# Optimization experiments

Measured on AMD Instinct MI355X. Metric: run time of the kernel, lower is better.

Reference implementation:

```python
import jax, jax.numpy as jnp
import numpy as np

# Model dims
B, S, D = 1, 768, 256          # batch, seq_len, d_model
H, KD = 8, 256                 # num_heads, key_dim
DH = KD // H                   # head_dim = 32
BS, NR, W, G = 64, 3, 3, 1     # block_size, num_rand_blocks, window_size, global_tokens
NEG = -1e9


def _build_sparse_indices(seed=0):
    """Replicates _create_sparse_attention_mask (sparse branch) with numpy.
    Returns (attn_indices [S, M] int32 clamped >=0, blocked_mask [1,1,S,M] float32)."""
    nb = S // BS  # num_blocks (S divisible by BS here)
    rng = np.random.RandomState(seed)
    r = np.arange(nb)
    # window pairs |i - j| <= W
    ii, jj = np.meshgrid(r, r, indexing='ij')
    win = np.abs(ii - jj) <= W
    window_pairs = np.stack([ii[win], jj[win]], axis=1)
    # global: every block -> first G blocks; first G blocks -> every block
    g = np.arange(G)
    glob_to = np.stack([np.repeat(r, G), np.tile(g, nb)], axis=1)
    glob_from = np.stack([np.repeat(g, nb), np.tile(r, G)], axis=1)
    # random pairs
    rand_pairs = rng.randint(0, nb, size=(NR * nb, 2))
    allp = np.concatenate([window_pairs, glob_to, glob_from, rand_pairs], axis=0)
    uniq = np.unique(allp[:, 0] * nb + allp[:, 1])  # sorted unique (row, col)
    rows, cols = uniq // nb, uniq % nb
    max_row = int(np.max(np.bincount(rows, minlength=nb)))
    M = max_row * BS  # padded neighbor-token width (= S when a global block is dense)
    idx = np.full((nb, M), -1, dtype=np.int64)
    for b in range(nb):
        cs = cols[rows == b]
        toks = (cs[:, None] * BS + np.arange(BS)[None, :]).reshape(-1)
        idx[b, :toks.size] = toks
    tok_idx = idx[np.arange(S) // BS]  # expand per-block rows to per-token rows [S, M]
    mask = np.where(tok_idx >= 0, 0.0, NEG).astype(np.float32)
    return np.maximum(tok_idx, 0).astype(np.int32), mask[None, None]


def setup_inputs() -> dict:
    key = jax.random.key(0)
    ks = jax.random.split(key, 8)

    def dense_w(k, fi, fo):  # glorot-uniform like keras Dense
        lim = float(np.sqrt(6.0 / (fi + fo)))
        return jax.random.uniform(k, (fi, fo), jnp.float32, -lim, lim)

    attn_indices, blocked_mask = _build_sparse_indices()
    return {
        'query': jax.random.normal(ks[0], (B, S, D), jnp.float32),
        'value': jax.random.normal(ks[1], (B, S, D), jnp.float32),
        'key_in': jax.random.normal(ks[2], (B, S, D), jnp.float32),
        'Wq': dense_w(ks[3], D, KD), 'bq': jnp.zeros((KD,), jnp.float32),
        'Wk': dense_w(ks[4], D, KD), 'bk': jnp.zeros((KD,), jnp.float32),
        'Wv': dense_w(ks[5], D, KD), 'bv': jnp.zeros((KD,), jnp.float32),
        'Wo': dense_w(ks[6], KD, D), 'bo': jnp.zeros((D,), jnp.float32),
        'attn_indices': jnp.asarray(attn_indices),
        'blocked_mask': jnp.asarray(blocked_mask),
    }


def reference(query, value, key_in, Wq, bq, Wk, bk, Wv, bv, Wo, bo, attn_indices, blocked_mask):
    q = query @ Wq + bq
    k = key_in @ Wk + bk
    v = value @ Wv + bv

    def split_heads(x):  # [B,S,KD] -> [B*H,S,DH]
        return x.reshape(B, S, H, DH).transpose(0, 2, 1, 3).reshape(B * H, S, DH)

    q = split_heads(q) * (DH ** -0.5)
    k = split_heads(k)
    v = split_heads(v)

    # gather sparse neighbor tokens (indices shared across batch*heads)
    k_g = jnp.take(k, attn_indices, axis=1)  # [BH, S, M, DH]
    v_g = jnp.take(v, attn_indices, axis=1)  # [BH, S, M, DH]

    scores = jnp.einsum('bnd,bnmd->bnm', q, k_g)  # [BH, S, M]
    M = attn_indices.shape[1]
    scores = scores.reshape(B, H, S, M) + blocked_mask  # pad positions -> -1e9
    probs = jax.nn.softmax(scores, axis=-1)

    ctx = jnp.einsum('bnm,bnmd->bnd', probs.reshape(B * H, S, M), v_g)  # [BH,S,DH]
    ctx = ctx.reshape(B, H, S, DH).transpose(0, 2, 1, 3).reshape(B, S, KD)
    out = ctx @ Wo + bo
    return out, scores, attn_indices
```

## Files before the change

### kernel.cpp

```cpp
#include <hip/hip_runtime.h>
#include <math.h>

#define SQ 768
#define DMODEL 256
#define NH 8
#define DHD 32
#define NB 12
#define QSCALE 0.1767766952966369f
#define PSHIFT 8.0f

__global__ __launch_bounds__(256) void proj3(
    const float* __restrict__ query, const float* __restrict__ value,
    const float* __restrict__ key_in,
    const float* __restrict__ Wq, const float* __restrict__ bq,
    const float* __restrict__ Wk, const float* __restrict__ bk,
    const float* __restrict__ Wv, const float* __restrict__ bv,
    const float* __restrict__ bo, float* __restrict__ outbuf,
    const int* __restrict__ aidx, float* __restrict__ idx_out,
    float* __restrict__ qhp, float* __restrict__ khp, float* __restrict__ vhp)
{
    const int j = threadIdx.x;

    {
        const int bidf = blockIdx.y * 96 + blockIdx.x;
        const int i0 = (bidf * 256 + j) * 8;
        int4 a = *(const int4*)&aidx[i0];
        int4 b = *(const int4*)&aidx[i0 + 4];
        *(float4*)&idx_out[i0] =
            make_float4((float)a.x, (float)a.y, (float)a.z, (float)a.w);
        *(float4*)&idx_out[i0 + 4] =
            make_float4((float)b.x, (float)b.y, (float)b.z, (float)b.w);
    }

    const int s0 = blockIdx.x * 8;
    const int w  = blockIdx.y;

    if (w == 0) {
        const float bb = bo[j];
        #pragma unroll
        for (int r = 0; r < 8; ++r)
            outbuf[(s0 + r) * DMODEL + j] = bb;
    }

    const float *X, *W, *bias; float* outp; float scale;
    if (w == 0)      { X = query;  W = Wq; bias = bq; outp = qhp; scale = QSCALE; }
    else if (w == 1) { X = key_in; W = Wk; bias = bk; outp = khp; scale = 1.0f; }
    else             { X = value;  W = Wv; bias = bv; outp = vhp; scale = 1.0f; }

    __shared__ __align__(16) float xs[8][DMODEL];
    {
        float* xsf = &xs[0][0];
        const float* Xp = X + s0 * DMODEL;
        const int i0 = j * 8;
        *(float4*)&xsf[i0]     = *(const float4*)&Xp[i0];
        *(float4*)&xsf[i0 + 4] = *(const float4*)&Xp[i0 + 4];
    }
    __syncthreads();

    const int j0 = (j & 127) * 2;
    const int r0 = (j >> 7) * 4;

    float acc[4][2] = {};
    #pragma unroll 2
    for (int k4 = 0; k4 < DMODEL / 4; ++k4) {
        float4 x0 = *(const float4*)&xs[r0 + 0][k4 * 4];
        float4 x1 = *(const float4*)&xs[r0 + 1][k4 * 4];
        float4 x2 = *(const float4*)&xs[r0 + 2][k4 * 4];
        float4 x3 = *(const float4*)&xs[r0 + 3][k4 * 4];
        const float xr[4][4] = {
            {x0.x, x0.y, x0.z, x0.w}, {x1.x, x1.y, x1.z, x1.w},
            {x2.x, x2.y, x2.z, x2.w}, {x3.x, x3.y, x3.z, x3.w}};
        #pragma unroll
        for (int kk = 0; kk < 4; ++kk) {
            const float2 wv = *(const float2*)&W[(k4 * 4 + kk) * DMODEL + j0];
            #pragma unroll
            for (int i = 0; i < 4; ++i) {
                acc[i][0] = fmaf(xr[i][kk], wv.x, acc[i][0]);
                acc[i][1] = fmaf(xr[i][kk], wv.y, acc[i][1]);
            }
        }
    }

    const float2 bb = *(const float2*)&bias[j0];
    const int h = j0 >> 5, d = j0 & 31;
    #pragma unroll
    for (int i = 0; i < 4; ++i) {
        float2 o;
        o.x = (acc[i][0] + bb.x) * scale;
        o.y = (acc[i][1] + bb.y) * scale;
        *(float2*)&outp[h * (SQ * DHD) + (s0 + r0 + i) * DHD + d] = o;
    }
}

__global__ __launch_bounds__(512) void attn2(
    const float* __restrict__ qh, const float* __restrict__ kh,
    const float* __restrict__ vh, const int* __restrict__ aidx,
    const float* __restrict__ mask, const float* __restrict__ Wo,
    float* __restrict__ scores_out, float* __restrict__ out, int M)
{
    __shared__ __align__(16) float Ks[2][2][32][68];
    __shared__ __align__(16) float Vs[2][2][64][36];
    __shared__ __align__(16) float Ps[2][64][33];
    __shared__ float dot0s[32];
    __shared__ float invL[32];

    const int b    = blockIdx.x;
    const int half = blockIdx.y;
    const int h    = blockIdx.z;
    const int s0b  = b * 64;
    const int s0   = s0b + half * 32;
    const int tid  = threadIdx.x;
    const int u    = tid >> 8;
    const int utid = tid & 255;
    const int NCH2 = M / 128;

    const int qrt = (utid & 15) * 2;
    const int qct = (utid >> 4) * 4;
    const int pr  = utid & 31;
    const int pd  = (utid >> 5) * 4;
    const int c   = utid & 63;
    const int dg  = utid >> 6;
    const int d4a = dg * 4;
    const int d4b = 16 + dg * 4;

    const float* mrow = &mask[s0b * M];
    const int*   arow = &aidx[s0b * M];
    float*       srow = &scores_out[(h * SQ + s0) * M];

    float qr0[32], qr1[32];
    {
        const float* qp = &qh[(h * SQ + s0 + qrt) * DHD];
        #pragma unroll
        for (int d4 = 0; d4 < DHD; d4 += 4) {
            float4 a  = *(const float4*)&qp[d4];
            float4 b4 = *(const float4*)&qp[DHD + d4];
            qr0[d4] = a.x;  qr0[d4+1] = a.y;  qr0[d4+2] = a.z;  qr0[d4+3] = a.w;
            qr1[d4] = b4.x; qr1[d4+1] = b4.y; qr1[d4+2] = b4.z; qr1[d4+3] = b4.w;
        }
    }

    if (tid < 16) {
        const float* k0 = &kh[h * SQ * DHD];
        float a0 = 0.f, a1 = 0.f;
        #pragma unroll
        for (int d = 0; d < DHD; ++d) {
            const float kv = k0[d];
            a0 = fmaf(qr0[d], kv, a0);
            a1 = fmaf(qr1[d], kv, a1);
        }
        dot0s[qrt] = a0; dot0s[qrt + 1] = a1;
    }

    float mv_cur = mrow[(u * NCH2) * 64];
    bool  val_cur = mv_cur > -0.5f;
    if (val_cur) {
        const int t0 = arow[(u * NCH2) * 64];
        const float* kp = &kh[(h * SQ + t0 + c) * DHD];
        const float* vp = &vh[(h * SQ + t0 + c) * DHD];
        float4 ka = *(const float4*)&kp[d4a];
        float4 kb = *(const float4*)&kp[d4b];
        Ks[u][0][d4a+0][c] = ka.x; Ks[u][0][d4a+1][c] = ka.y;
        Ks[u][0][d4a+2][c] = ka.z; Ks[u][0][d4a+3][c] = ka.w;
        Ks[u][0][d4b+0][c] = kb.x; Ks[u][0][d4b+1][c] = kb.y;
        Ks[u][0][d4b+2][c] = kb.z; Ks[u][0][d4b+3][c] = kb.w;
        *(float4*)&Vs[u][0][c][d4a] = *(const float4*)&vp[d4a];
        *(float4*)&Vs[u][0][c][d4b] = *(const float4*)&vp[d4b];
    }
    __syncthreads();

    float4 acc = make_float4(0.f, 0.f, 0.f, 0.f);
    float rps = 0.f;
    int cur = 0;

    for (int ci = 0; ci < NCH2; ++ci) {
        const int m0 = (u * NCH2 + ci) * 64;

        bool  val_nxt = false;
        float mv_nxt  = 0.f;
        float4 ka, kb, va, vb;
        if (ci + 1 < NCH2) {
            mv_nxt  = mrow[m0 + 64];
            val_nxt = mv_nxt > -0.5f;
            if (val_nxt) {
                const int t0 = arow[m0 + 64];
                const float* kp = &kh[(h * SQ + t0 + c) * DHD];
                const float* vp = &vh[(h * SQ + t0 + c) * DHD];
                ka = *(const float4*)&kp[d4a];
                kb = *(const float4*)&kp[d4b];
                va = *(const float4*)&vp[d4a];
                vb = *(const float4*)&vp[d4b];
            }
        }

        if (val_cur) {
            const float* Kb = &Ks[u][cur][0][qct];
            float sc[2][4] = {};
            #pragma unroll
            for (int kk = 0; kk < 32; ++kk) {
                float4 b4 = *(const float4*)&Kb[kk * 68];
                sc[0][0] = fmaf(qr0[kk], b4.x, sc[0][0]);
                sc[0][1] = fmaf(qr0[kk], b4.y, sc[0][1]);
                sc[0][2] = fmaf(qr0[kk], b4.z, sc[0][2]);
                sc[0][3] = fmaf(qr0[kk], b4.w, sc[0][3]);
                sc[1][0] = fmaf(qr1[kk], b4.x, sc[1][0]);
                sc[1][1] = fmaf(qr1[kk], b4.y, sc[1][1]);
                sc[1][2] = fmaf(qr1[kk], b4.z, sc[1][2]);
                sc[1][3] = fmaf(qr1[kk], b4.w, sc[1][3]);
            }
            #pragma unroll
            for (int i = 0; i < 2; ++i) {
                *(float4*)&srow[(qrt + i) * M + m0 + qct] =
                    make_float4(sc[i][0], sc[i][1], sc[i][2], sc[i][3]);
                #pragma unroll
                for (int jj = 0; jj < 4; ++jj)
                    Ps[u][qct + jj][qrt + i] = __expf(sc[i][jj] - PSHIFT);
            }
        } else {
            #pragma unroll
            for (int i = 0; i < 8; ++i) {
                const int e = utid + i * 256;
                const int r = e >> 6, cc = e & 63;
                srow[r * M + m0 + cc] = dot0s[r] + mv_cur;
            }
        }

        if (val_nxt) {
            Ks[u][cur^1][d4a+0][c] = ka.x; Ks[u][cur^1][d4a+1][c] = ka.y;
            Ks[u][cur^1][d4a+2][c] = ka.z; Ks[u][cur^1][d4a+3][c] = ka.w;
            Ks[u][cur^1][d4b+0][c] = kb.x; Ks[u][cur^1][d4b+1][c] = kb.y;
            Ks[u][cur^1][d4b+2][c] = kb.z; Ks[u][cur^1][d4b+3][c] = kb.w;
            *(float4*)&Vs[u][cur^1][c][d4a] = va;
            *(float4*)&Vs[u][cur^1][c][d4b] = vb;
        }
        __syncthreads();

        if (val_cur) {
            const float (*Vb)[36] = Vs[u][cur];
            #pragma unroll 4
            for (int cc2 = 0; cc2 < 64; ++cc2) {
                const float p = Ps[u][cc2][pr];
                float4 v = *(const float4*)&Vb[cc2][pd];
                acc.x = fmaf(p, v.x, acc.x);
                acc.y = fmaf(p, v.y, acc.y);
                acc.z = fmaf(p, v.z, acc.z);
                acc.w = fmaf(p, v.w, acc.w);
                if (utid < 32) rps += p;
            }
        }
        __syncthreads();

        val_cur = val_nxt; mv_cur = mv_nxt; cur ^= 1;
    }

    *(float4*)&Vs[u][0][pr][pd] = acc;
    if (utid < 32) (&Ps[1][0][0])[u * 32 + utid] = rps;
    __syncthreads();

    if (tid < 32) {
        const float pt = (&Ps[1][0][0])[tid] + (&Ps[1][0][0])[32 + tid];
        invL[tid] = 1.0f / pt;
    }
    __syncthreads();

    float* ctxn = &Ks[0][0][0][0];
    #pragma unroll
    for (int g = 0; g < 2; ++g) {
        const int idx = tid + g * 512;
        const int r = idx >> 5, d = idx & 31;
        ctxn[r * 36 + d] = (Vs[0][0][r][d] + Vs[1][0][r][d]) * invL[r];
    }
    __syncthreads();

    {
        const int jc = tid & 255, rg = tid >> 8;
        float wo[32];
        #pragma unroll
        for (int k = 0; k < 32; ++k)
            wo[k] = Wo[(h * DHD + k) * DMODEL + jc];
        for (int rr = rg * 16; rr < rg * 16 + 16; ++rr) {
            float a = 0.f;
            #pragma unroll
            for (int k4 = 0; k4 < 8; ++k4) {
                float4 cv = *(const float4*)&ctxn[rr * 36 + k4 * 4];
                a = fmaf(cv.x, wo[k4 * 4 + 0], a);
                a = fmaf(cv.y, wo[k4 * 4 + 1], a);
                a = fmaf(cv.z, wo[k4 * 4 + 2], a);
                a = fmaf(cv.w, wo[k4 * 4 + 3], a);
            }
            atomicAdd(&out[(s0 + rr) * DMODEL + jc], a);
        }
    }
}

extern "C" void kernel_launch(void* const* d_in, const int* in_sizes, int n_in,
                              void* d_out, int out_size, void* d_ws, size_t ws_size,
                              hipStream_t stream)
{
    const float* query  = (const float*)d_in[0];
    const float* value  = (const float*)d_in[1];
    const float* key_in = (const float*)d_in[2];
    const float* Wq = (const float*)d_in[3];
    const float* bq = (const float*)d_in[4];
    const float* Wk = (const float*)d_in[5];
    const float* bk = (const float*)d_in[6];
    const float* Wv = (const float*)d_in[7];
    const float* bv = (const float*)d_in[8];
    const float* Wo = (const float*)d_in[9];
    const float* bo = (const float*)d_in[10];
    const int*   aidx = (const int*)d_in[11];
    const float* mask = (const float*)d_in[12];

    const int M = in_sizes[11] / SQ;

    float* out        = (float*)d_out;
    float* scores_out = out + SQ * DMODEL;
    float* idx_out    = scores_out + NH * SQ * M;

    float* ws  = (float*)d_ws;
    float* qhp = ws;
    float* khp = qhp + NH * SQ * DHD;
    float* vhp = khp + NH * SQ * DHD;

    proj3<<<dim3(96, 3), 256, 0, stream>>>(
        query, value, key_in, Wq, bq, Wk, bk, Wv, bv,
        bo, out, aidx, idx_out, qhp, khp, vhp);

    attn2<<<dim3(NB, 2, NH), 512, 0, stream>>>(
        qhp, khp, vhp, aidx, mask, Wo, scores_out, out, M);
}
```

Measured before the change: 55.57 us.

## Register-tile the P·V product and accumulate row sums during the exp pass

Ps is now stored row-major as [32][68], so probabilities are written as float4 and read back as float4. The P·V loop becomes a 2x8 register tile: each thread owns 2 query rows and 8 head dims over a 16-column slice of the chunk. This replaces one P load per 4 FMAs with vectorized P and V loads reused across 16 FMAs. Row sums are accumulated in the exp pass instead of by a 32-thread serial branch. The cost is a larger cross-thread reduction at the end, over 8 partial contexts and 32 row-sum slices, plus more accumulator registers per thread.

```diff
diff --git a/kernel.cpp b/kernel.cpp
--- a/kernel.cpp
+++ b/kernel.cpp
@@ -100,7 +100,7 @@
 {
     __shared__ __align__(16) float Ks[2][2][32][68];
     __shared__ __align__(16) float Vs[2][2][64][36];
-    __shared__ __align__(16) float Ps[2][64][33];
+    __shared__ __align__(16) float Ps[2][32][68];
     __shared__ float dot0s[32];
     __shared__ float invL[32];
 
@@ -116,12 +116,13 @@
 
     const int qrt = (utid & 15) * 2;
     const int qct = (utid >> 4) * 4;
-    const int pr  = utid & 31;
-    const int pd  = (utid >> 5) * 4;
+    const int rp  = utid & 15;
+    const int dg  = (utid >> 4) & 3;
+    const int cg  = utid >> 6;
     const int c   = utid & 63;
-    const int dg  = utid >> 6;
-    const int d4a = dg * 4;
-    const int d4b = 16 + dg * 4;
+    const int sg  = utid >> 6;
+    const int d4a = sg * 4;
+    const int d4b = 16 + sg * 4;
 
     const float* mrow = &mask[s0b * M];
     const int*   arow = &aidx[s0b * M];
@@ -168,8 +169,9 @@
     }
     __syncthreads();
 
-    float4 acc = make_float4(0.f, 0.f, 0.f, 0.f);
-    float rps = 0.f;
+    float4 acc0a = make_float4(0.f,0.f,0.f,0.f), acc0b = acc0a;
+    float4 acc1a = acc0a, acc1b = acc0a;
+    float rps0 = 0.f, rps1 = 0.f;
     int cur = 0;
 
     for (int ci = 0; ci < NCH2; ++ci) {
@@ -207,13 +209,23 @@
                 sc[1][2] = fmaf(qr1[kk], b4.z, sc[1][2]);
                 sc[1][3] = fmaf(qr1[kk], b4.w, sc[1][3]);
             }
-            #pragma unroll
-            for (int i = 0; i < 2; ++i) {
-                *(float4*)&srow[(qrt + i) * M + m0 + qct] =
-                    make_float4(sc[i][0], sc[i][1], sc[i][2], sc[i][3]);
-                #pragma unroll
-                for (int jj = 0; jj < 4; ++jj)
-                    Ps[u][qct + jj][qrt + i] = __expf(sc[i][jj] - PSHIFT);
+            {
+                *(float4*)&srow[(qrt + 0) * M + m0 + qct] =
+                    make_float4(sc[0][0], sc[0][1], sc[0][2], sc[0][3]);
+                float4 e;
+                e.x = __expf(sc[0][0] - PSHIFT); e.y = __expf(sc[0][1] - PSHIFT);
+                e.z = __expf(sc[0][2] - PSHIFT); e.w = __expf(sc[0][3] - PSHIFT);
+                *(float4*)&Ps[u][qrt + 0][qct] = e;
+                rps0 += (e.x + e.y) + (e.z + e.w);
+            }
+            {
+                *(float4*)&srow[(qrt + 1) * M + m0 + qct] =
+                    make_float4(sc[1][0], sc[1][1], sc[1][2], sc[1][3]);
+                float4 e;
+                e.x = __expf(sc[1][0] - PSHIFT); e.y = __expf(sc[1][1] - PSHIFT);
+                e.z = __expf(sc[1][2] - PSHIFT); e.w = __expf(sc[1][3] - PSHIFT);
+                *(float4*)&Ps[u][qrt + 1][qct] = e;
+                rps1 += (e.x + e.y) + (e.z + e.w);
             }
         } else {
             #pragma unroll
@@ -236,15 +248,38 @@
 
         if (val_cur) {
             const float (*Vb)[36] = Vs[u][cur];
-            #pragma unroll 4
-            for (int cc2 = 0; cc2 < 64; ++cc2) {
-                const float p = Ps[u][cc2][pr];
-                float4 v = *(const float4*)&Vb[cc2][pd];
-                acc.x = fmaf(p, v.x, acc.x);
-                acc.y = fmaf(p, v.y, acc.y);
-                acc.z = fmaf(p, v.z, acc.z);
-                acc.w = fmaf(p, v.w, acc.w);
-                if (utid < 32) rps += p;
+            const float* Pr0 = &Ps[u][2 * rp][0];
+            const float* Pr1 = &Ps[u][2 * rp + 1][0];
+            const int c0 = cg * 16;
+            const int dd = dg * 8;
+            #pragma unroll
+            for (int k = 0; k < 4; ++k) {
+                float4 pa = *(const float4*)&Pr0[c0 + k * 4];
+                float4 pb = *(const float4*)&Pr1[c0 + k * 4];
+                const float pav[4] = {pa.x, pa.y, pa.z, pa.w};
+                const float pbv[4] = {pb.x, pb.y, pb.z, pb.w};
+                #pragma unroll
+                for (int t = 0; t < 4; ++t) {
+                    const int cc2 = c0 + k * 4 + t;
+                    float4 v0 = *(const float4*)&Vb[cc2][dd];
+                    float4 v1 = *(const float4*)&Vb[cc2][dd + 4];
+                    acc0a.x = fmaf(pav[t], v0.x, acc0a.x);
+                    acc0a.y = fmaf(pav[t], v0.y, acc0a.y);
+                    acc0a.z = fmaf(pav[t], v0.z, acc0a.z);
+                    acc0a.w = fmaf(pav[t], v0.w, acc0a.w);
+                    acc0b.x = fmaf(pav[t], v1.x, acc0b.x);
+                    acc0b.y = fmaf(pav[t], v1.y, acc0b.y);
+                    acc0b.z = fmaf(pav[t], v1.z, acc0b.z);
+                    acc0b.w = fmaf(pav[t], v1.w, acc0b.w);
+                    acc1a.x = fmaf(pbv[t], v0.x, acc1a.x);
+                    acc1a.y = fmaf(pbv[t], v0.y, acc1a.y);
+                    acc1a.z = fmaf(pbv[t], v0.z, acc1a.z);
+                    acc1a.w = fmaf(pbv[t], v0.w, acc1a.w);
+                    acc1b.x = fmaf(pbv[t], v1.x, acc1b.x);
+                    acc1b.y = fmaf(pbv[t], v1.y, acc1b.y);
+                    acc1b.z = fmaf(pbv[t], v1.z, acc1b.z);
+                    acc1b.w = fmaf(pbv[t], v1.w, acc1b.w);
+                }
             }
         }
         __syncthreads();
@@ -252,22 +287,39 @@
         val_cur = val_nxt; mv_cur = mv_nxt; cur ^= 1;
     }
 
-    *(float4*)&Vs[u][0][pr][pd] = acc;
-    if (utid < 32) (&Ps[1][0][0])[u * 32 + utid] = rps;
+    float* vacc = &Vs[0][0][0][0];
+    float* rsum = &Ps[0][0][0];
+    {
+        const int s = u * 4 + cg;
+        float* base = vacc + (s * 32 + 2 * rp) * 36 + dg * 8;
+        *(float4*)&base[0]  = acc0a; *(float4*)&base[4]  = acc0b;
+        *(float4*)&base[36] = acc1a; *(float4*)&base[40] = acc1b;
+        const int qg = utid >> 4;
+        rsum[(u * 16 + qg) * 32 + qrt]     = rps0;
+        rsum[(u * 16 + qg) * 32 + qrt + 1] = rps1;
+    }
     __syncthreads();
 
     if (tid < 32) {
-        const float pt = (&Ps[1][0][0])[tid] + (&Ps[1][0][0])[32 + tid];
+        float pt = 0.f;
+        #pragma unroll
+        for (int s2 = 0; s2 < 32; ++s2) pt += rsum[s2 * 32 + tid];
         invL[tid] = 1.0f / pt;
     }
     __syncthreads();
 
     float* ctxn = &Ks[0][0][0][0];
-    #pragma unroll
-    for (int g = 0; g < 2; ++g) {
-        const int idx = tid + g * 512;
-        const int r = idx >> 5, d = idx & 31;
-        ctxn[r * 36 + d] = (Vs[0][0][r][d] + Vs[1][0][r][d]) * invL[r];
+    if (tid < 256) {
+        const int r = tid & 31, dq = tid >> 5;
+        float4 sum = make_float4(0.f, 0.f, 0.f, 0.f);
+        #pragma unroll
+        for (int s = 0; s < 8; ++s) {
+            float4 v = *(const float4*)&vacc[(s * 32 + r) * 36 + dq * 4];
+            sum.x += v.x; sum.y += v.y; sum.z += v.z; sum.w += v.w;
+        }
+        const float il = invL[r];
+        sum.x *= il; sum.y *= il; sum.z *= il; sum.w *= il;
+        *(float4*)&ctxn[r * 36 + dq * 4] = sum;
     }
     __syncthreads();
 
```

Measured after the change: 51.97 us. 1.07x faster.
